# Kernel optimization log

Measured on AMD Instinct MI355X. Metric: run time of the kernel, lower is better.

## Reference

```python
import jax, jax.numpy as jnp
import numpy as np

B, A, C = 16, 16384, 81
TOP_K = 50
CONF_THRESH = 0.5
IOU_THRESH = 0.5
VAR0, VAR1 = 0.1, 0.2          # cfg['variance']
IMG_HW = 1.0                   # cfg['min_dim']/img_size = 320/320
MIN_SIZE = 0.0
NEG = -jnp.inf


def setup_inputs() -> dict:
    key = jax.random.key(0)
    k1, k2, k3 = jax.random.split(key, 3)
    conf_preds = jax.random.uniform(k1, (B, A, C), dtype=jnp.float32)
    loc_delta = jax.random.normal(k2, (B, A, 4), dtype=jnp.float32)
    anchors = jax.random.uniform(k3, (A, 4), dtype=jnp.float32)  # cxcywh priors in [0,1)
    return {"conf_preds": conf_preds, "loc_delta": loc_delta, "anchors": anchors}


def _decode_clip(loc, anchors):
    # SSD decode: cxcy = prior_cxcy + loc_xy*v0*prior_wh ; wh = prior_wh*exp(loc_wh*v1)
    cxcy = anchors[..., :2] + loc[..., :2] * VAR0 * anchors[..., 2:]
    wh = anchors[..., 2:] * jnp.exp(loc[..., 2:] * VAR1)
    x1y1 = cxcy - wh * 0.5
    x2y2 = x1y1 + wh
    boxes = jnp.concatenate([x1y1, x2y2], axis=-1)  # [..., 4] xyxy
    return jnp.clip(boxes, 0.0, IMG_HW)            # clip_boxes_to_image((1,1))


def _nms_single(boxes, s):
    # boxes: [A,4] xyxy, s: [A] scores with invalid entries already at -inf.
    # Greedy NMS, fixed TOP_K iterations (torchvision semantics: suppress iou > thresh).
    areas = (boxes[:, 2] - boxes[:, 0]) * (boxes[:, 3] - boxes[:, 1])

    def step(s, _):
        i = jnp.argmax(s)
        take = s[i] > NEG
        b = boxes[i]
        xx1 = jnp.maximum(b[0], boxes[:, 0])
        yy1 = jnp.maximum(b[1], boxes[:, 1])
        xx2 = jnp.minimum(b[2], boxes[:, 2])
        yy2 = jnp.minimum(b[3], boxes[:, 3])
        inter = jnp.maximum(xx2 - xx1, 0.0) * jnp.maximum(yy2 - yy1, 0.0)
        iou = inter / (areas[i] + areas - inter)
        s = jnp.where(take & (iou > IOU_THRESH), NEG, s)
        s = s.at[i].set(NEG)  # guarantee progress
        return s, (i, take)

    _, (idx, take) = jax.lax.scan(step, s, None, length=TOP_K)
    return idx, take  # [TOP_K] int, [TOP_K] bool


def reference(conf_preds, loc_delta, anchors):
    boxes = _decode_clip(loc_delta, anchors)                # [B,A,4]
    conf = jnp.transpose(conf_preds, (0, 2, 1))             # [B,C,A]
    # remove_small_boxes(min_size=0) as a mask (all-true here, kept for fidelity)
    w = boxes[..., 2] - boxes[..., 0]
    h = boxes[..., 3] - boxes[..., 1]
    valid = (w >= MIN_SIZE) & (h >= MIN_SIZE)               # [B,A]
    masked = jnp.where((conf > CONF_THRESH) & valid[:, None, :], conf, NEG)  # [B,C,A]

    sg = jax.lax.stop_gradient
    nms_c = jax.vmap(_nms_single, in_axes=(None, 0))        # over classes
    nms_bc = jax.vmap(nms_c, in_axes=(0, 0))                # over batch
    idx, take = nms_bc(sg(boxes), sg(masked))               # [B,C,K]

    scores_sel = jnp.take_along_axis(conf, idx, axis=2)     # [B,C,K]
    b_idx = jnp.arange(boxes.shape[0])[:, None, None]
    boxes_sel = boxes[b_idx, idx]                           # [B,C,K,4]
    preds = jnp.concatenate([
        jnp.where(take, scores_sel, 0.0)[..., None],
        jnp.where(take[..., None], boxes_sel, 0.0),
    ], axis=-1)                                             # [B,C,K,5]
    return preds
```

## Files before the change

kernel.cpp:

```cpp
#include <hip/hip_runtime.h>
#include <math.h>

#define NB 16
#define NA 16384
#define NC 81
#define TOPK 50
#define NBK 255
#define TRC 1024
#define NEGF (-__builtin_inff())
#define SUPC 0.5000000298023223876953125

typedef unsigned long long ull;

#define WS_CONFT_OFF  ((size_t)4194304)
#define WS_FULL  (WS_CONFT_OFF + (size_t)NB * NC * NA)

__device__ __forceinline__ bool iou_gt_half(float inter, float den) {
    return fmaf(den, -0.5f, inter) > den * 0x1p-25f;
}

__device__ __forceinline__ unsigned enc8(float v) {
    unsigned e = 0xFFu;
    if (v > 0.5f) {
        unsigned d = 255u - ((__float_as_uint(v) >> 15) & 0xFFu);
        e = (d > 254u) ? 254u : d;
    }
    return e;
}

__device__ __forceinline__ void decode_body(int i, const float* __restrict__ loc,
                                            const float* __restrict__ anc,
                                            float* __restrict__ boxes) {
#pragma clang fp contract(off)
    int a = i & (NA - 1);
    float4 an = ((const float4*)anc)[a];
    float4 ld = ((const float4*)loc)[i];
    float cx = an.x + (ld.x * 0.1f) * an.z;
    float cy = an.y + (ld.y * 0.1f) * an.w;
    float w = an.z * (float)exp((double)(ld.z * 0.2f));
    float h = an.w * (float)exp((double)(ld.w * 0.2f));
    float x1 = cx - w * 0.5f;
    float y1 = cy - h * 0.5f;
    float x2 = x1 + w;
    float y2 = y1 + h;
    x1 = fminf(fmaxf(x1, 0.f), 1.f);
    y1 = fminf(fmaxf(y1, 0.f), 1.f);
    x2 = fminf(fmaxf(x2, 0.f), 1.f);
    y2 = fminf(fmaxf(y2, 0.f), 1.f);
    ((float4*)boxes)[i] = make_float4(x1, y1, x2, y2);
}

__global__ __launch_bounds__(256) void decode_k(const float* __restrict__ loc,
                                                const float* __restrict__ anc,
                                                float* __restrict__ boxes) {
    int i = blockIdx.x * 256 + threadIdx.x;
    if (i < NB * NA) decode_body(i, loc, anc, boxes);
}

#define TSLAB 256
__global__ __launch_bounds__(256) void prep_k(const float* __restrict__ conf,
                                              const float* __restrict__ loc,
                                              const float* __restrict__ anc,
                                              float* __restrict__ boxes,
                                              unsigned char* __restrict__ confT) {
    __shared__ unsigned char code[TSLAB * NC];
    const int t = threadIdx.x;
    if (blockIdx.z == 1) {
        int i = (blockIdx.x + 64 * blockIdx.y) * 256 + t;
        if (i < NB * NA) decode_body(i, loc, anc, boxes);
        return;
    }
    const int b = blockIdx.y, slab = blockIdx.x;
    const float4* src = (const float4*)(conf + ((size_t)b * NA + (size_t)slab * TSLAB) * NC);
    for (int i = t; i < (TSLAB * NC) / 4; i += 256) {
        float4 v = src[i];
        unsigned wrd = enc8(v.x) | (enc8(v.y) << 8) | (enc8(v.z) << 16) | (enc8(v.w) << 24);
        *(unsigned*)&code[4 * i] = wrd;
    }
    __syncthreads();
    const int lane = t & 63, wv = t >> 6;
    for (int c = wv; c < NC; c += 4) {
        unsigned v = 0u;
#pragma unroll
        for (int j = 0; j < 4; ++j)
            v |= (unsigned)code[(4 * lane + j) * NC + c] << (8 * j);
        *(unsigned*)(confT + ((size_t)b * NC + c) * NA + (size_t)slab * TSLAB + 4 * lane) = v;
    }
}

#define HIST16(Q)                                                          \
    do {                                                                   \
        unsigned wrds_[4] = {(Q).x, (Q).y, (Q).z, (Q).w};                  \
        _Pragma("unroll")                                                  \
        for (int m_ = 0; m_ < 4; ++m_) {                                   \
            _Pragma("unroll")                                              \
            for (int k_ = 0; k_ < 4; ++k_) {                               \
                unsigned bk_ = (wrds_[m_] >> (8 * k_)) & 0xFFu;            \
                if (bk_ != 0xFFu) atomicAdd(&s_hist[wv][bk_], 1u);         \
            }                                                              \
        }                                                                  \
    } while (0)

#define SCAT16(Q, BA)                                                      \
    do {                                                                   \
        unsigned wrds_[4] = {(Q).x, (Q).y, (Q).z, (Q).w};                  \
        _Pragma("unroll")                                                  \
        for (int m_ = 0; m_ < 4; ++m_) {                                   \
            _Pragma("unroll")                                              \
            for (int k_ = 0; k_ < 4; ++k_) {                               \
                int bk_ = (int)((wrds_[m_] >> (8 * k_)) & 0xFFu);          \
                if (bk_ >= trLo && bk_ < trHi)                             \
                    s_ix[atomicAdd(&s_cur[bk_], 1u)] =                     \
                        (unsigned short)((BA) + 4 * m_ + k_);              \
            }                                                              \
        }                                                                  \
    } while (0)

__global__ __launch_bounds__(256, 8) void nmsB9_k(const unsigned char* __restrict__ confT,
                                                  const float* __restrict__ conf,
                                                  const float* __restrict__ boxes,
                                                  float* __restrict__ out) {
#pragma clang fp contract(off)
    const int blk = blockIdx.x;
    const int b = blk / NC, c = blk - b * NC;
    const int t = threadIdx.x;
    const int lane = t & 63, wv = t >> 6;

    __shared__ unsigned short s_ix[TRC];
    __shared__ unsigned s_off[NBK + 1];
    __shared__ unsigned s_hist[4][NBK + 2];
    __shared__ unsigned s_cur[NBK];
    __shared__ unsigned s_wsum[4];
    __shared__ float4 s_abox[TOPK];
    __shared__ float s_aarea[TOPK];
    __shared__ float4 s_cbox[256];
    __shared__ unsigned long long s_kill[4];
    __shared__ int s_ctrl[16];

    const uint4* row16 = (const uint4*)(confT + ((size_t)b * NC + c) * NA);
    const float* cp = conf + ((size_t)b * NA) * NC + c;
    const float4* bb = (const float4*)boxes + (size_t)b * NA;
    float* orow = out + ((size_t)b * NC + c) * (TOPK * 5);

    for (int i = t; i < 4 * (NBK + 2); i += 256) ((unsigned*)s_hist)[i] = 0u;
    if (t == 0) { s_ctrl[0] = 0; s_ctrl[8] = 0; s_ctrl[12] = 0; }
    __syncthreads();

#pragma unroll
    for (int r = 0; r < 4; ++r) {
        uint4 q = row16[t + 256 * r];
        HIST16(q);
    }
    __syncthreads();

    unsigned cnt = 0u;
    if (t < NBK) {
        cnt = s_hist[0][t] + s_hist[1][t] + s_hist[2][t] + s_hist[3][t];
        atomicMax(&s_ctrl[8], (int)cnt);
    }
    unsigned v = cnt;
#pragma unroll
    for (int off = 1; off < 64; off <<= 1) {
        unsigned o = __shfl_up(v, off);
        if (lane >= off) v += o;
    }
    if (lane == 63) s_wsum[wv] = v;
    __syncthreads();
    unsigned basep = 0u;
    for (int w2 = 0; w2 < wv; ++w2) basep += s_wsum[w2];
    v += basep;
    if (t < NBK) s_off[t + 1] = v;
    if (t == 0) s_off[0] = 0u;
    __syncthreads();

    if (s_ctrl[8] <= TRC) {
        while (true) {
            if (t == 0) {
                int lo = s_ctrl[12];
                int hi = lo;
                while (hi < NBK && s_off[hi + 1] - s_off[lo] <= (unsigned)TRC) hi++;
                s_ctrl[13] = hi;
            }
            __syncthreads();
            const int trLo = s_ctrl[12], trHi = s_ctrl[13];
            const unsigned tbase = s_off[trLo], tend = s_off[trHi];
            if (tbase == tend) break;
            for (int i = trLo + t; i < trHi; i += 256) s_cur[i] = s_off[i] - tbase;
            __syncthreads();
#pragma unroll
            for (int r = 0; r < 4; ++r) {
                uint4 q = row16[t + 256 * r];
                SCAT16(q, 16 * (t + 256 * r));
            }
            if (t == 0) s_ctrl[7] = trLo;
            __syncthreads();

            while (true) {
                if (t == 0) {
                    int bp = s_ctrl[7];
                    int mode;
                    if (bp >= trHi || s_off[bp] >= tend) {
                        mode = 2;
                    } else {
                        unsigned pos = s_off[bp] - tbase;
                        int bpl = bp;
                        unsigned q = pos;
                        for (int w = 0; w < 4; ++w) {
                            s_ctrl[2 + w] = (int)q;
                            while (bpl < trHi && (s_off[bpl + 1] - tbase - q) <= 64u) bpl++;
                            q = (bpl < trHi) ? s_off[bpl] - tbase : tend - tbase;
                        }
                        s_ctrl[6] = (int)q;
                        s_ctrl[7] = bpl;
                        mode = 0;
                        if (q == pos) {
                            mode = 1;
                            s_ctrl[9] = (int)pos;
                            s_ctrl[10] = (int)(s_off[bp + 1] - tbase);
                            s_ctrl[7] = bp + 1;
                        }
                    }
                    s_ctrl[11] = mode;
                }
                __syncthreads();
                const int mode = s_ctrl[11];
                if (mode == 2) break;
                const int nacc0 = s_ctrl[0];

                if (mode == 0) {
                    const unsigned q0 = (unsigned)s_ctrl[2 + wv];
                    const unsigned q1 = (unsigned)s_ctrl[3 + wv];
                    const int mw = (int)(q1 - q0);
                    const bool valid = lane < mw;
                    int ii = (int)q0 + lane; if (ii > TRC - 1) ii = TRC - 1;
                    int a = valid ? (int)s_ix[ii] : 0;
                    float4 bxv = bb[a];
                    if (!valid) bxv = make_float4(0.f, 0.f, 0.f, 0.f);
                    s_cbox[wv * 64 + lane] = bxv;
                    float mar = (bxv.z - bxv.x) * (bxv.w - bxv.y);
                    bool kill = !valid;
                    for (int j = 0; j < nacc0; ++j) {
                        float4 ab = s_abox[j];
                        float aa = s_aarea[j];
                        float xx1 = fmaxf(ab.x, bxv.x), yy1 = fmaxf(ab.y, bxv.y);
                        float xx2 = fminf(ab.z, bxv.z), yy2 = fminf(ab.w, bxv.w);
                        float iw = fmaxf(xx2 - xx1, 0.f), ih = fmaxf(yy2 - yy1, 0.f);
                        float inter = iw * ih;
                        float den = (aa + mar) - inter;
                        if (iou_gt_half(inter, den)) kill = true;
                    }
                    unsigned long long km = __ballot(kill);
                    if (lane == 0) s_kill[wv] = km;
                    __syncthreads();

                    if (wv == 0) {
                        int na = nacc0;
                        for (int cc = 0; cc < 4 && na < TOPK; ++cc) {
                            const unsigned e0 = (unsigned)s_ctrl[2 + cc];
                            const unsigned e1 = (unsigned)s_ctrl[3 + cc];
                            const int mc = (int)(e1 - e0);
                            if (mc <= 0) continue;
                            unsigned long long alive = ~s_kill[cc];
                            if (mc < 64) alive &= (1ull << mc) - 1ull;
                            int jj = (int)e0 + lane; if (jj > TRC - 1) jj = TRC - 1;
                            int aj = (lane < mc) ? (int)s_ix[jj] : 0;
                            float myscore = cp[(size_t)aj * NC];
                            float4 mybx = s_cbox[cc * 64 + lane];
                            float mar2 = (mybx.z - mybx.x) * (mybx.w - mybx.y);
                            for (int j = nacc0; j < na && alive; ++j) {
                                float4 ab = s_abox[j];
                                float aa = s_aarea[j];
                                float xx1 = fmaxf(ab.x, mybx.x), yy1 = fmaxf(ab.y, mybx.y);
                                float xx2 = fminf(ab.z, mybx.z), yy2 = fminf(ab.w, mybx.w);
                                float iw = fmaxf(xx2 - xx1, 0.f), ih = fmaxf(yy2 - yy1, 0.f);
                                float inter = iw * ih;
                                float den = (aa + mar2) - inter;
                                bool sup = iou_gt_half(inter, den);
                                alive &= ~__ballot(sup);
                            }
                            unsigned long long mykey =
                                ((unsigned long long)__float_as_uint(myscore) << 32) |
                                (unsigned)(16383 - aj);
                            while (alive && na < TOPK) {
                                unsigned long long kk = ((alive >> lane) & 1ull) ? mykey : 0ull;
                                int src = lane;
                                for (int off = 32; off; off >>= 1) {
                                    unsigned long long ok = __shfl_xor(kk, off);
                                    int osrc = __shfl_xor(src, off);
                                    if (ok > kk) { kk = ok; src = osrc; }
                                }
                                float4 wb = s_cbox[cc * 64 + src];
                                float wscore = __shfl(myscore, src);
                                float war = (wb.z - wb.x) * (wb.w - wb.y);
                                if (lane == 0) {
                                    orow[na * 5 + 0] = wscore;
                                    orow[na * 5 + 1] = wb.x; orow[na * 5 + 2] = wb.y;
                                    orow[na * 5 + 3] = wb.z; orow[na * 5 + 4] = wb.w;
                                    s_abox[na] = wb;
                                    s_aarea[na] = war;
                                }
                                na++;
                                alive &= ~(1ull << src);
                                if (alive) {
                                    float xx1 = fmaxf(wb.x, mybx.x), yy1 = fmaxf(wb.y, mybx.y);
                                    float xx2 = fminf(wb.z, mybx.z), yy2 = fminf(wb.w, mybx.w);
                                    float iw = fmaxf(xx2 - xx1, 0.f), ih = fmaxf(yy2 - yy1, 0.f);
                                    float inter = iw * ih;
                                    float den = (war + mar2) - inter;
                                    bool sup = iou_gt_half(inter, den);
                                    alive &= ~__ballot(sup);
                                }
                            }
                        }
                        if (lane == 0) s_ctrl[0] = na;
                    }
                    __syncthreads();
                } else {
                    const int e0 = s_ctrl[9], e1 = s_ctrl[10];
                    if (wv == 0) {
                        int na = s_ctrl[0];
                        while (na < TOPK) {
                            unsigned long long bk = 0ull; int bpos = 0;
                            for (int i = e0 + lane; i < e1; i += 64) {
                                int av = (int)s_ix[i];
                                if (av != 0xFFFF) {
                                    float vv = cp[(size_t)av * NC];
                                    unsigned long long k =
                                        ((unsigned long long)__float_as_uint(vv) << 32) |
                                        (unsigned)(16383 - av);
                                    if (k > bk) { bk = k; bpos = i; }
                                }
                            }
                            for (int off = 32; off; off >>= 1) {
                                unsigned long long ok = __shfl_xor(bk, off);
                                int op = __shfl_xor(bpos, off);
                                if (ok > bk) { bk = ok; bpos = op; }
                            }
                            if (bk == 0ull) break;
                            int a = (int)s_ix[bpos];
                            float wscore = __uint_as_float((unsigned)(bk >> 32));
                            if (lane == 0) s_ix[bpos] = 0xFFFFu;
                            float4 wb = bb[a];
                            float war = (wb.z - wb.x) * (wb.w - wb.y);
                            bool sup = false;
                            if (lane < na) {
                                float4 ab = s_abox[lane];
                                float aa = s_aarea[lane];
                                float xx1 = fmaxf(ab.x, wb.x), yy1 = fmaxf(ab.y, wb.y);
                                float xx2 = fminf(ab.z, wb.z), yy2 = fminf(ab.w, wb.w);
                                float iw = fmaxf(xx2 - xx1, 0.f), ih = fmaxf(yy2 - yy1, 0.f);
                                float inter = iw * ih;
                                float den = (aa + war) - inter;
                                sup = iou_gt_half(inter, den);
                            }
                            if (__ballot(sup) == 0ull) {
                                if (lane == 0) {
                                    orow[na * 5 + 0] = wscore;
                                    orow[na * 5 + 1] = wb.x; orow[na * 5 + 2] = wb.y;
                                    orow[na * 5 + 3] = wb.z; orow[na * 5 + 4] = wb.w;
                                    s_abox[na] = wb;
                                    s_aarea[na] = war;
                                }
                                na++;
                            }
                        }
                        if (lane == 0) s_ctrl[0] = na;
                    }
                    __syncthreads();
                }
                if (s_ctrl[0] >= TOPK) break;
            }
            if (s_ctrl[0] >= TOPK || trHi >= NBK) break;
            if (t == 0) s_ctrl[12] = trHi;
            __syncthreads();
        }
    } else {
        float hi = 1.0f, delta = 0.02f;
        while (true) {
            if (s_ctrl[0] >= TOPK || hi <= 0.5f) break;
            float lo = fmaxf(hi - delta, 0.5f);
            if (t == 0) s_ctrl[1] = 0;
            __syncthreads();
            for (int a = t; a < NA; a += 256) {
                float vv = cp[(size_t)a * NC];
                if (vv > lo && vv <= hi) {
                    int p = atomicAdd(&s_ctrl[1], 1);
                    if (p < TRC) s_ix[p] = (unsigned short)a;
                }
            }
            __syncthreads();
            int m = s_ctrl[1];
            if (m > TRC) { delta *= 0.5f; continue; }
            if (wv == 0) {
                int na = s_ctrl[0];
                while (na < TOPK) {
                    unsigned long long bk = 0ull; int bpos = 0;
                    for (int i = lane; i < m; i += 64) {
                        int av = (int)s_ix[i];
                        if (av != 0xFFFF) {
                            float vv = cp[(size_t)av * NC];
                            unsigned long long k =
                                ((unsigned long long)__float_as_uint(vv) << 32) |
                                (unsigned)(16383 - av);
                            if (k > bk) { bk = k; bpos = i; }
                        }
                    }
                    for (int off = 32; off; off >>= 1) {
                        unsigned long long ok = __shfl_xor(bk, off);
                        int op = __shfl_xor(bpos, off);
                        if (ok > bk) { bk = ok; bpos = op; }
                    }
                    if (bk == 0ull) break;
                    int a = (int)s_ix[bpos];
                    float wscore = __uint_as_float((unsigned)(bk >> 32));
                    if (lane == 0) s_ix[bpos] = 0xFFFFu;
                    float4 wb = bb[a];
                    float war = (wb.z - wb.x) * (wb.w - wb.y);
                    bool sup = false;
                    if (lane < na) {
                        float4 ab = s_abox[lane];
                        float aa = s_aarea[lane];
                        float xx1 = fmaxf(ab.x, wb.x), yy1 = fmaxf(ab.y, wb.y);
                        float xx2 = fminf(ab.z, wb.z), yy2 = fminf(ab.w, wb.w);
                        float iw = fmaxf(xx2 - xx1, 0.f), ih = fmaxf(yy2 - yy1, 0.f);
                        float inter = iw * ih;
                        float den = (aa + war) - inter;
                        sup = iou_gt_half(inter, den);
                    }
                    if (__ballot(sup) == 0ull) {
                        if (lane == 0) {
                            orow[na * 5 + 0] = wscore;
                            orow[na * 5 + 1] = wb.x; orow[na * 5 + 2] = wb.y;
                            orow[na * 5 + 3] = wb.z; orow[na * 5 + 4] = wb.w;
                            s_abox[na] = wb;
                            s_aarea[na] = war;
                        }
                        na++;
                    }
                }
                if (lane == 0) s_ctrl[0] = na;
            }
            __syncthreads();
            hi = lo;
        }
    }

    __syncthreads();
    const int naF = s_ctrl[0];
    for (int z = naF * 5 + t; z < TOPK * 5; z += 256) orow[z] = 0.f;
}

#define OTHREADS 1024
#define OCAP 10240
#define OJMAX 10

__global__ __launch_bounds__(OTHREADS) void nms_old_k(const float* __restrict__ conf,
                                                      const float* __restrict__ boxes,
                                                      float* __restrict__ out) {
#pragma clang fp contract(off)
    const int blk = blockIdx.x;
    const int b = blk / NC, c = blk - b * NC;
    const int t = threadIdx.x;
    const int lane = t & 63, wid = t >> 6;
    __shared__ float s_val[OCAP];
    __shared__ unsigned short s_idx[OCAP];
    __shared__ float s_ps[2][16];
    __shared__ int s_pa[2][16];
    __shared__ int s_n;
    if (t == 0) s_n = 0;
    __syncthreads();
    const float* cp = conf + ((size_t)b * NA) * NC + c;
    float v[NA / OTHREADS];
#pragma unroll
    for (int r = 0; r < NA / OTHREADS; ++r)
        v[r] = cp[(size_t)(r * OTHREADS + t) * NC];
#pragma unroll
    for (int r = 0; r < NA / OTHREADS; ++r) {
        int a = r * OTHREADS + t;
        bool alive = v[r] > 0.5f;
        unsigned long long m = __ballot(alive);
        int cnt = __popcll(m);
        int base = 0;
        if (lane == 0 && cnt) base = atomicAdd(&s_n, cnt);
        base = __shfl(base, 0);
        if (alive) {
            int p = base + __popcll(m & ((1ull << lane) - 1));
            if (p < OCAP) { s_val[p] = v[r]; s_idx[p] = (unsigned short)a; }
        }
    }
    __syncthreads();
    int n = s_n; if (n > OCAP) n = OCAP;
    const int jn = (n + OTHREADS - 1) / OTHREADS;
    const float4* bb = (const float4*)boxes + (size_t)b * NA;
    float sc[OJMAX]; float4 bx[OJMAX]; int ia[OJMAX];
#pragma unroll
    for (int j = 0; j < OJMAX; ++j) {
        sc[j] = NEGF; ia[j] = 0x7fffffff; bx[j] = make_float4(0.f, 0.f, 0.f, 0.f);
        int p = j * OTHREADS + t;
        if (p < n) { sc[j] = s_val[p]; ia[j] = (int)s_idx[p]; bx[j] = bb[ia[j]]; }
    }
    float* orow = out + (size_t)blk * (TOPK * 5);
    int k = 0;
    for (; k < TOPK; ++k) {
        float ms = NEGF; int ma = 0x7fffffff;
#pragma unroll
        for (int j = 0; j < OJMAX; ++j) {
            if (j < jn) {
                bool better = (sc[j] > ms) || (sc[j] == ms && ia[j] < ma);
                ms = better ? sc[j] : ms;
                ma = better ? ia[j] : ma;
            }
        }
#pragma unroll
        for (int off = 32; off; off >>= 1) {
            float os = __shfl_xor(ms, off);
            int oa = __shfl_xor(ma, off);
            if (os > ms || (os == ms && oa < ma)) { ms = os; ma = oa; }
        }
        int pb = k & 1;
        if (lane == 0) { s_ps[pb][wid] = ms; s_pa[pb][wid] = ma; }
        __syncthreads();
        float wsv = NEGF; int wa = 0x7fffffff;
#pragma unroll
        for (int w = 0; w < 16; ++w) {
            float os = s_ps[pb][w]; int oa = s_pa[pb][w];
            if (os > wsv || (os == wsv && oa < wa)) { wsv = os; wa = oa; }
        }
        if (!(wsv > NEGF)) break;
        float4 wb = bb[wa];
        float warea = (wb.z - wb.x) * (wb.w - wb.y);
        if (t == 0) {
            orow[k * 5 + 0] = wsv;
            orow[k * 5 + 1] = wb.x; orow[k * 5 + 2] = wb.y;
            orow[k * 5 + 3] = wb.z; orow[k * 5 + 4] = wb.w;
        }
#pragma unroll
        for (int j = 0; j < OJMAX; ++j) {
            if (j < jn) {
                float xx1 = fmaxf(wb.x, bx[j].x);
                float yy1 = fmaxf(wb.y, bx[j].y);
                float xx2 = fminf(wb.z, bx[j].z);
                float yy2 = fminf(wb.w, bx[j].w);
                float iw = fmaxf(xx2 - xx1, 0.f);
                float ih = fmaxf(yy2 - yy1, 0.f);
                float inter = iw * ih;
                float aj = (bx[j].z - bx[j].x) * (bx[j].w - bx[j].y);
                float denom = (warea + aj) - inter;
                bool supp = ((double)inter > (double)denom * SUPC) || (ia[j] == wa);
                if (supp) sc[j] = NEGF;
            }
        }
    }
    for (int z = k * 5 + t; z < TOPK * 5; z += OTHREADS) orow[z] = 0.f;
}

extern "C" void kernel_launch(void* const* d_in, const int* in_sizes, int n_in,
                              void* d_out, int out_size, void* d_ws, size_t ws_size,
                              hipStream_t stream) {
    const float* conf = (const float*)d_in[0];
    const float* loc  = (const float*)d_in[1];
    const float* anc  = (const float*)d_in[2];
    float* boxes = (float*)d_ws;

    if (ws_size >= WS_FULL) {
        unsigned char* confT = (unsigned char*)((char*)d_ws + WS_CONFT_OFF);
        dim3 tg(NA / TSLAB, NB, 2);
        prep_k<<<tg, 256, 0, stream>>>(conf, loc, anc, boxes, confT);
        nmsB9_k<<<NB * NC, 256, 0, stream>>>(confT, conf, boxes, (float*)d_out);
    } else {
        decode_k<<<(NB * NA + 255) / 256, 256, 0, stream>>>(loc, anc, boxes);
        nms_old_k<<<NB * NC, OTHREADS, 0, stream>>>(conf, boxes, (float*)d_out);
    }
}
```

Before: 193.6 us.

## Fuse decode into transpose blocks, enlarge candidate buffer, add early-exit and score caching

```diff
diff --git a/kernel.cpp b/kernel.cpp
--- a/kernel.cpp
+++ b/kernel.cpp
@@ -6,7 +6,7 @@
 #define NC 81
 #define TOPK 50
 #define NBK 255
-#define TRC 1024
+#define TRC 4096
 #define NEGF (-__builtin_inff())
 #define SUPC 0.5000000298023223876953125
 
@@ -65,12 +65,8 @@
                                               unsigned char* __restrict__ confT) {
     __shared__ unsigned char code[TSLAB * NC];
     const int t = threadIdx.x;
-    if (blockIdx.z == 1) {
-        int i = (blockIdx.x + 64 * blockIdx.y) * 256 + t;
-        if (i < NB * NA) decode_body(i, loc, anc, boxes);
-        return;
-    }
     const int b = blockIdx.y, slab = blockIdx.x;
+    decode_body(b * NA + slab * TSLAB + t, loc, anc, boxes);
     const float4* src = (const float4*)(conf + ((size_t)b * NA + (size_t)slab * TSLAB) * NC);
     for (int i = t; i < (TSLAB * NC) / 4; i += 256) {
         float4 v = src[i];
@@ -116,10 +112,10 @@
         }                                                                  \
     } while (0)
 
-__global__ __launch_bounds__(256, 8) void nmsB9_k(const unsigned char* __restrict__ confT,
-                                                  const float* __restrict__ conf,
-                                                  const float* __restrict__ boxes,
-                                                  float* __restrict__ out) {
+__global__ __launch_bounds__(256, 6) void nmsB10_k(const unsigned char* __restrict__ confT,
+                                                   const float* __restrict__ conf,
+                                                   const float* __restrict__ boxes,
+                                                   float* __restrict__ out) {
 #pragma clang fp contract(off)
     const int blk = blockIdx.x;
     const int b = blk / NC, c = blk - b * NC;
@@ -134,6 +130,7 @@
     __shared__ float4 s_abox[TOPK];
     __shared__ float s_aarea[TOPK];
     __shared__ float4 s_cbox[256];
+    __shared__ float s_cscore[256];
     __shared__ unsigned long long s_kill[4];
     __shared__ int s_ctrl[16];
 
@@ -142,15 +139,16 @@
     const float4* bb = (const float4*)boxes + (size_t)b * NA;
     float* orow = out + ((size_t)b * NC + c) * (TOPK * 5);
 
+    uint4 q0 = row16[t];
+    uint4 q1 = row16[t + 256];
+    uint4 q2 = row16[t + 512];
+    uint4 q3 = row16[t + 768];
+
     for (int i = t; i < 4 * (NBK + 2); i += 256) ((unsigned*)s_hist)[i] = 0u;
     if (t == 0) { s_ctrl[0] = 0; s_ctrl[8] = 0; s_ctrl[12] = 0; }
     __syncthreads();
 
-#pragma unroll
-    for (int r = 0; r < 4; ++r) {
-        uint4 q = row16[t + 256 * r];
-        HIST16(q);
-    }
+    HIST16(q0); HIST16(q1); HIST16(q2); HIST16(q3);
     __syncthreads();
 
     unsigned cnt = 0u;
@@ -228,18 +226,21 @@
                 const int nacc0 = s_ctrl[0];
 
                 if (mode == 0) {
-                    const unsigned q0 = (unsigned)s_ctrl[2 + wv];
-                    const unsigned q1 = (unsigned)s_ctrl[3 + wv];
-                    const int mw = (int)(q1 - q0);
+                    const unsigned q0c = (unsigned)s_ctrl[2 + wv];
+                    const unsigned q1c = (unsigned)s_ctrl[3 + wv];
+                    const int mw = (int)(q1c - q0c);
                     const bool valid = lane < mw;
-                    int ii = (int)q0 + lane; if (ii > TRC - 1) ii = TRC - 1;
+                    int ii = (int)q0c + lane; if (ii > TRC - 1) ii = TRC - 1;
                     int a = valid ? (int)s_ix[ii] : 0;
                     float4 bxv = bb[a];
+                    float sc = valid ? cp[(size_t)a * NC] : 0.f;
                     if (!valid) bxv = make_float4(0.f, 0.f, 0.f, 0.f);
                     s_cbox[wv * 64 + lane] = bxv;
+                    s_cscore[wv * 64 + lane] = sc;
                     float mar = (bxv.z - bxv.x) * (bxv.w - bxv.y);
                     bool kill = !valid;
                     for (int j = 0; j < nacc0; ++j) {
+                        if (__ballot(!kill) == 0ull) break;
                         float4 ab = s_abox[j];
                         float aa = s_aarea[j];
                         float xx1 = fmaxf(ab.x, bxv.x), yy1 = fmaxf(ab.y, bxv.y);
@@ -264,7 +265,7 @@
                             if (mc < 64) alive &= (1ull << mc) - 1ull;
                             int jj = (int)e0 + lane; if (jj > TRC - 1) jj = TRC - 1;
                             int aj = (lane < mc) ? (int)s_ix[jj] : 0;
-                            float myscore = cp[(size_t)aj * NC];
+                            float myscore = s_cscore[cc * 64 + lane];
                             float4 mybx = s_cbox[cc * 64 + lane];
                             float mar2 = (mybx.z - mybx.x) * (mybx.w - mybx.y);
                             for (int j = nacc0; j < na && alive; ++j) {
@@ -564,9 +565,9 @@
 
     if (ws_size >= WS_FULL) {
         unsigned char* confT = (unsigned char*)((char*)d_ws + WS_CONFT_OFF);
-        dim3 tg(NA / TSLAB, NB, 2);
+        dim3 tg(NA / TSLAB, NB);
         prep_k<<<tg, 256, 0, stream>>>(conf, loc, anc, boxes, confT);
-        nmsB9_k<<<NB * NC, 256, 0, stream>>>(confT, conf, boxes, (float*)d_out);
+        nmsB10_k<<<NB * NC, 256, 0, stream>>>(confT, conf, boxes, (float*)d_out);
     } else {
         decode_k<<<(NB * NA + 255) / 256, 256, 0, stream>>>(loc, anc, boxes);
         nms_old_k<<<NB * NC, OTHREADS, 0, stream>>>(conf, boxes, (float*)d_out);
```

New measurement: 200.6 us. +3.6%, slower.
